# Performance work log

Measured on AMD Instinct MI355X. Metric: run time of the kernel, lower is better.

## Reference

```python
import jax, jax.numpy as jnp
import numpy as np

N_NODES, N_EDGES, N_GRAPHS, H = 20000, 160000, 256, 128
EPS = 1e-5


def setup_inputs() -> dict:
    key = jax.random.key(0)
    it = iter(jax.random.split(key, 64))

    def nk():
        return next(it)

    def lin(fan_in, wshape, bshape):
        s = 1.0 / np.sqrt(fan_in)
        W = jax.random.uniform(nk(), wshape, jnp.float32, -s, s)
        b = jax.random.uniform(nk(), bshape, jnp.float32, -s, s)
        return W, b

    def bn_params(shape):
        g = 1.0 + 0.1 * jax.random.normal(nk(), shape, jnp.float32)
        b = 0.1 * jax.random.normal(nk(), shape, jnp.float32)
        m = 0.1 * jax.random.normal(nk(), shape, jnp.float32)
        v = jax.random.uniform(nk(), shape, jnp.float32, 0.5, 1.5)
        return g, b, m, v

    inp = {}
    inp["x"] = jax.random.normal(nk(), (N_NODES, 10), jnp.float32)
    inp["edge_attr"] = jax.random.normal(nk(), (N_EDGES, 3), jnp.float32)
    inp["edge_index"] = jax.random.randint(nk(), (2, N_EDGES), 0, N_NODES)
    inp["batch"] = jnp.sort(jax.random.randint(nk(), (N_NODES,), 0, N_GRAPHS))
    inp["W_node"], inp["b_node"] = lin(10, (10, H), (H,))
    inp["W_edge"], inp["b_edge"] = lin(3, (3, H), (H,))
    # 10 stacked CGConv layers: lin_f / lin_s each map [2H + H] -> H
    inp["Wf"], inp["bf"] = lin(3 * H, (10, 3 * H, H), (10, H))
    inp["Ws"], inp["bs"] = lin(3 * H, (10, 3 * H, H), (10, H))
    inp["bn_g"], inp["bn_b"], inp["bn_m"], inp["bn_v"] = bn_params((10, H))
    inp["W1"], inp["b1"] = lin(3 * H, (3 * H, 2 * H), (2 * H,))
    inp["bn1_g"], inp["bn1_b"], inp["bn1_m"], inp["bn1_v"] = bn_params((2 * H,))
    inp["W2"], inp["b2"] = lin(2 * H, (2 * H, H), (H,))
    inp["bn2_g"], inp["bn2_b"], inp["bn2_m"], inp["bn2_v"] = bn_params((H,))
    inp["W3"], inp["b3"] = lin(H, (H, H // 2), (H // 2,))
    inp["Wv"], inp["bv"] = lin(H // 2, (H // 2, 1), (1,))
    inp["W_en"], inp["b_en"] = lin(H // 2, (H // 2, 1), (1,))
    inp["Wd"], inp["bd"] = lin(H // 2, (H // 2, 1), (1,))
    inp["Wh"], inp["bh"] = lin(H // 2, (H // 2, 1), (1,))
    return inp


def reference(x, edge_attr, edge_index, batch, W_node, b_node, W_edge, b_edge,
              Wf, bf, Ws, bs, bn_g, bn_b, bn_m, bn_v,
              W1, b1, bn1_g, bn1_b, bn1_m, bn1_v,
              W2, b2, bn2_g, bn2_b, bn2_m, bn2_v,
              W3, b3, Wv, bv, W_en, b_en, Wd, bd, Wh, bh):
    h = jax.nn.relu(x @ W_node + b_node)             # [N, H]
    e = jax.nn.relu(edge_attr @ W_edge + b_edge)     # [E, H]
    src, dst = edge_index[0], edge_index[1]          # PyG: messages src -> dst
    n = h.shape[0]
    for i in range(10):  # fixed layer count, structurally distinct weights
        h_in = h
        z = jnp.concatenate([h[dst], h[src], e], axis=1)          # [E, 3H] = [x_i, x_j, e_ij]
        msg = jax.nn.sigmoid(z @ Wf[i] + bf[i]) * jax.nn.softplus(z @ Ws[i] + bs[i])
        h = h_in + jax.ops.segment_sum(msg, dst, num_segments=n)  # CGConv residual + add-aggr
        h = (h - bn_m[i]) * (bn_g[i] / jnp.sqrt(bn_v[i] + EPS)) + bn_b[i]  # BN (eval)
        h = jax.nn.relu(h)  # dropout is identity in eval
        if i % 2 == 1:
            h = h + h_in
    # global mean / max / add pooling over graphs
    s = jax.ops.segment_sum(h, batch, num_segments=N_GRAPHS)                     # [G, H]
    cnt = jax.ops.segment_sum(jnp.ones((n, 1), h.dtype), batch, num_segments=N_GRAPHS)
    mean = s / jnp.maximum(cnt, 1.0)
    mx = jax.ops.segment_max(h, batch, num_segments=N_GRAPHS)
    g = jnp.concatenate([mean, mx, s], axis=1)                                   # [G, 3H]
    g = jax.nn.relu((g @ W1 + b1 - bn1_m) * (bn1_g / jnp.sqrt(bn1_v + EPS)) + bn1_b)
    g = jax.nn.relu((g @ W2 + b2 - bn2_m) * (bn2_g / jnp.sqrt(bn2_v + EPS)) + bn2_b)
    g = jax.nn.relu(g @ W3 + b3)
    return (g @ Wv + bv, g @ W_en + b_en, g @ Wd + bd, g @ Wh + bh)
```

## Files before the change

### kernel.cpp

```cpp
#include <hip/hip_runtime.h>
#include <hip/hip_bf16.h>
#include <math.h>

#define NN 20000
#define NE 160000
#define NG 256
#define EPSV 1e-5f
#define NQB 2500

typedef short bf16x8 __attribute__((ext_vector_type(8)));
typedef unsigned short u16x8 __attribute__((ext_vector_type(8)));
typedef float f32x4 __attribute__((ext_vector_type(4)));

__device__ __forceinline__ unsigned short f2bf(float f){
  unsigned int u = __float_as_uint(f);
  unsigned int r = (u + 0x7fffu + ((u>>16)&1u)) >> 16;
  return (unsigned short)r;
}
__device__ __forceinline__ float bf2f(unsigned short h){
  return __uint_as_float(((unsigned int)h) << 16);
}
__device__ __forceinline__ float fastmsg(float f, float sv){
  float sg = __builtin_amdgcn_rcpf(1.0f + __expf(-f));
  float sp = fmaxf(sv, 0.0f) + __logf(1.0f + __expf(-fabsf(sv)));
  return sg * sp;
}

__global__ __launch_bounds__(256) void k_hist(const int* __restrict__ ei, int* __restrict__ deg){
  int e = blockIdx.x*256 + threadIdx.x;
  if (e < NE) atomicAdd(&deg[ei[NE+e]], 1);
}
__global__ __launch_bounds__(1024) void k_scan(const int* __restrict__ deg,
                                               int* __restrict__ start, int* __restrict__ cur){
  __shared__ int part[1024];
  int t = threadIdx.x;
  int base = t*20;
  int s = 0;
  for (int j=0;j<20;j++){ int i = base+j; if (i<NN) s += deg[i]; }
  part[t] = s; __syncthreads();
  for (int off=1; off<1024; off<<=1){
    int v = (t >= off) ? part[t-off] : 0;
    __syncthreads();
    part[t] += v;
    __syncthreads();
  }
  int run = (t>0) ? part[t-1] : 0;
  for (int j=0;j<20;j++){
    int i = base+j;
    if (i<NN){ start[i] = run; cur[i] = run; run += deg[i]; }
  }
}
__global__ __launch_bounds__(256) void k_scatter(
    const int* __restrict__ ei, const float* __restrict__ eattr,
    int* __restrict__ cur, int2* __restrict__ esd, float* __restrict__ ea_s){
  int e = blockIdx.x*256 + threadIdx.x;
  if (e >= NE) return;
  int d = ei[NE+e];
  int p = atomicAdd(&cur[d], 1);
  esd[p] = make_int2(ei[e], d);
  ea_s[p*3+0] = eattr[e*3+0];
  ea_s[p*3+1] = eattr[e*3+1];
  ea_s[p*3+2] = eattr[e*3+2];
}

__global__ __launch_bounds__(256) void k_edge_frag(
    const float* __restrict__ ea_s, const float* __restrict__ W_edge,
    const float* __restrict__ b_edge, unsigned short* __restrict__ E_frag)
{
  int idx = blockIdx.x*256 + threadIdx.x;
  if (idx >= 640000) return;
  int g = idx >> 6, l = idx & 63;
  int row = g*16 + (l&15);
  float a0 = ea_s[row*3+0], a1 = ea_s[row*3+1], a2 = ea_s[row*3+2];
  int cbase = (l>>4)*8;
  unsigned short* dst = E_frag + (size_t)g*4096 + l*8;
  #pragma unroll
  for (int ks=0;ks<4;ks++){
    u16x8 hv, lv;
    #pragma unroll
    for (int j=0;j<8;j++){
      int c = cbase + ks*32 + j;
      float v = fmaf(a0, W_edge[c], fmaf(a1, W_edge[128+c], fmaf(a2, W_edge[256+c], b_edge[c])));
      v = fmaxf(v, 0.0f);
      unsigned short hi = f2bf(v);
      hv[j] = hi;
      lv[j] = f2bf(v - bf2f(hi));
    }
    *(u16x8*)(dst + ks*512) = hv;
    *(u16x8*)(dst + 2048 + ks*512) = lv;
  }
}

__global__ __launch_bounds__(256) void k_pack_w(
    const float* __restrict__ Wf, const float* __restrict__ Ws,
    unsigned short* __restrict__ Wpk_hi, unsigned short* __restrict__ Wpk_md,
    unsigned short* __restrict__ Wpk_lo)
{
  int idx = blockIdx.x*256 + threadIdx.x;
  if (idx >= 122880) return;
  int l = idx & 63, ks = (idx>>6)&3, nt = (idx>>8)&7;
  int m = idx >> 11;
  int blk = m % 3, gL = m / 3;
  int g = gL & 1, L = gL >> 1;
  const float* src = (g ? Ws : Wf) + (size_t)L*384*128;
  size_t off = (size_t)m*16384 + (nt*4+ks)*512 + l*8;
  int col = nt*16 + (l&15), k0 = ks*32 + (l>>4)*8;
  #pragma unroll
  for (int j=0;j<8;j++){
    float w = src[(size_t)(blk*128 + k0 + j)*128 + col];
    unsigned short hi = f2bf(w);
    float r1 = w - bf2f(hi);
    unsigned short md = f2bf(r1);
    float r2 = r1 - bf2f(md);
    Wpk_hi[off+j] = hi;
    Wpk_md[off+j] = md;
    Wpk_lo[off+j] = f2bf(r2);
  }
}

__global__ __launch_bounds__(256) void k_embed_node(
    const float* __restrict__ x, const float* __restrict__ W, const float* __restrict__ b,
    float* __restrict__ h, float* __restrict__ hacc)
{
  int i = blockIdx.x*256 + threadIdx.x;
  if (i >= NN*128) return;
  int n = i >> 7, c = i & 127;
  float acc = b[c];
  const float* xr = x + n*10;
  #pragma unroll
  for (int k=0;k<10;k++) acc = fmaf(xr[k], W[k*128+c], acc);
  acc = fmaxf(acc, 0.0f);
  h[i] = acc; hacc[i] = acc;
}

__global__ __launch_bounds__(512,2) void k_nodeproj_mfma(
    const float* __restrict__ h,
    const unsigned short* __restrict__ Wpk_hi, const unsigned short* __restrict__ Wpk_md,
    const unsigned short* __restrict__ Wpk_lo,
    const float* __restrict__ bfv, const float* __restrict__ bsv,
    float* __restrict__ Pd, float* __restrict__ Ps)
{
  __shared__ unsigned short wsm[32768];
  int bid = blockIdx.x;
  int m_idx = bid / 157, nblk = bid - m_idx*157;
  int mm = (m_idx==0)?0:(m_idx==1)?1:(m_idx==2)?3:4;
  int t = threadIdx.x;
  {
    const unsigned short* s0 = Wpk_hi + (size_t)mm*16384;
    const unsigned short* s1 = Wpk_md + (size_t)mm*16384;
    #pragma unroll
    for (int ii=0; ii<4; ii++){
      int o = (t + ii*512)*8;
      *(u16x8*)(wsm + o)         = *(const u16x8*)(s0 + o);
      *(u16x8*)(wsm + 16384 + o) = *(const u16x8*)(s1 + o);
    }
  }
  __syncthreads();
  int l = t & 63, w = t >> 6;
  int nb = nblk*128 + w*16;
  if (nb + 16 > NN) return;
  const float* hb = h + (size_t)(nb + (l&15))*128 + (l>>4)*8;
  bf16x8 ah[4], am[4], al[4];
  #pragma unroll
  for (int ks=0;ks<4;ks++){
    #pragma unroll
    for (int j=0;j<8;j++){
      float v = hb[ks*32 + j];
      unsigned short x0 = f2bf(v);
      float r1 = v - bf2f(x0);
      unsigned short x1 = f2bf(r1);
      float r2 = r1 - bf2f(x1);
      ah[ks][j] = (short)x0; am[ks][j] = (short)x1; al[ks][j] = (short)f2bf(r2);
    }
  }
  const unsigned short* wl = Wpk_lo + (size_t)mm*16384 + l*8;
  float* OUT = (m_idx & 1) ? Ps : Pd;
  int sel = (m_idx >= 2) ? 1 : 0;
  const float* bias = (m_idx==0) ? bfv : (m_idx==2) ? bsv : nullptr;
  int col0 = l & 15, rg = (l>>4)*4;
  #pragma unroll
  for (int nt=0; nt<8; nt++){
    f32x4 c = {0.f,0.f,0.f,0.f};
    #pragma unroll
    for (int ks=0;ks<4;ks++){
      int fo = (nt*4+ks)*512 + l*8;
      bf16x8 bh = *(const bf16x8*)(wsm + fo);
      bf16x8 bm = *(const bf16x8*)(wsm + 16384 + fo);
      bf16x8 bl = *(const bf16x8*)(wl + (nt*4+ks)*512);
      c = __builtin_amdgcn_mfma_f32_16x16x32_bf16(al[ks], bh, c, 0,0,0);
      c = __builtin_amdgcn_mfma_f32_16x16x32_bf16(am[ks], bm, c, 0,0,0);
      c = __builtin_amdgcn_mfma_f32_16x16x32_bf16(ah[ks], bl, c, 0,0,0);
      c = __builtin_amdgcn_mfma_f32_16x16x32_bf16(am[ks], bh, c, 0,0,0);
      c = __builtin_amdgcn_mfma_f32_16x16x32_bf16(ah[ks], bm, c, 0,0,0);
      c = __builtin_amdgcn_mfma_f32_16x16x32_bf16(ah[ks], bh, c, 0,0,0);
    }
    float bb = bias ? bias[nt*16+col0] : 0.0f;
    #pragma unroll
    for (int r=0;r<4;r++)
      OUT[(size_t)(nb+rg+r)*256 + (nt*16+col0)*2 + sel] = c[r] + bb;
  }
}

template<bool PRE>
__global__ __launch_bounds__(256,4) void k_edge_mfma(
    const float* __restrict__ ea_s, const float* __restrict__ W_edge,
    const float* __restrict__ b_edge,
    const unsigned short* __restrict__ E_frag,
    const unsigned short* __restrict__ Wpk_hi,
    const unsigned short* __restrict__ Wpk_md,
    const int2* __restrict__ esd,
    const float* __restrict__ Pd, const float* __restrict__ Ps,
    float* __restrict__ hacc)
{
  __shared__ float wlds[512];
  __shared__ unsigned short bfr[16384];
  int bid = blockIdx.x;
  int q = bid / NQB, eg = bid - q*NQB;
  int t = threadIdx.x;
  if (!PRE)
    for (int i=t;i<512;i+=256) wlds[i] = (i<384)? W_edge[i] : b_edge[i-384];
  #pragma unroll
  for (int ii=0; ii<8; ii++){
    int idx = t + ii*256;
    int f = idx >> 6;
    int off = (idx & 63) * 8;
    int g = f >> 4, term = (f>>3)&1, ntl = (f>>2)&1, ks = f&3;
    const unsigned short* src = (term ? Wpk_md : Wpk_hi)
        + (size_t)(g?5:2)*16384 + (size_t)((((q*2+ntl)*4+ks)*512) + off);
    *(u16x8*)(bfr + f*512 + off) = *(const u16x8*)src;
  }
  __syncthreads();
  int l = t & 63, w = t >> 6;
  int e0 = eg*64;
  bf16x8 ah[4], al[4];
  if (PRE) {
    const unsigned short* ef = E_frag + (size_t)(eg*4 + w)*4096 + l*8;
    #pragma unroll
    for (int ks=0;ks<4;ks++){
      ah[ks] = *(const bf16x8*)(ef + ks*512);
      al[ks] = *(const bf16x8*)(ef + 2048 + ks*512);
    }
  } else {
    int row_edge = e0 + w*16 + (l&15);
    float a0 = ea_s[row_edge*3+0], a1 = ea_s[row_edge*3+1], a2 = ea_s[row_edge*3+2];
    int cbase = (l>>4)*8;
    #pragma unroll
    for (int ks=0;ks<4;ks++){
      #pragma unroll
      for (int j=0;j<8;j++){
        int c = cbase + ks*32 + j;
        float v = fmaf(a0, wlds[c], fmaf(a1, wlds[128+c], fmaf(a2, wlds[256+c], wlds[384+c])));
        v = fmaxf(v, 0.0f);
        unsigned short hi = f2bf(v);
        ah[ks][j] = (short)hi;
        al[ks][j] = (short)f2bf(v - bf2f(hi));
      }
    }
  }
  f32x4 accf[2], accs[2];
  #pragma unroll
  for (int ntl=0; ntl<2; ntl++){
    f32x4 cf = {0.f,0.f,0.f,0.f}, cs = {0.f,0.f,0.f,0.f};
    #pragma unroll
    for (int ks=0; ks<4; ks++){
      bf16x8 bh = *(const bf16x8*)(bfr + ((0<<4)|(0<<3)|(ntl<<2)|ks)*512 + l*8);
      bf16x8 bm = *(const bf16x8*)(bfr + ((0<<4)|(1<<3)|(ntl<<2)|ks)*512 + l*8);
      cf = __builtin_amdgcn_mfma_f32_16x16x32_bf16(ah[ks], bh, cf, 0,0,0);
      cf = __builtin_amdgcn_mfma_f32_16x16x32_bf16(ah[ks], bm, cf, 0,0,0);
      cf = __builtin_amdgcn_mfma_f32_16x16x32_bf16(al[ks], bh, cf, 0,0,0);
      bf16x8 sh = *(const bf16x8*)(bfr + ((1<<4)|(0<<3)|(ntl<<2)|ks)*512 + l*8);
      bf16x8 sm = *(const bf16x8*)(bfr + ((1<<4)|(1<<3)|(ntl<<2)|ks)*512 + l*8);
      cs = __builtin_amdgcn_mfma_f32_16x16x32_bf16(ah[ks], sh, cs, 0,0,0);
      cs = __builtin_amdgcn_mfma_f32_16x16x32_bf16(ah[ks], sm, cs, 0,0,0);
      cs = __builtin_amdgcn_mfma_f32_16x16x32_bf16(al[ks], sh, cs, 0,0,0);
    }
    accf[ntl] = cf; accs[ntl] = cs;
  }
  int eb = e0 + w*16, col0 = l & 15, rg = (l>>4)*4;
  int cA = (q*2+0)*16 + col0;
  int cB = (q*2+1)*16 + col0;
  int prev_d = -1;
  float m0 = 0.f, m1 = 0.f;
  float2 pd0, pd1;
  #pragma unroll
  for (int r=0;r<4;r++){
    int p = eb + rg + r;
    int2 sd = esd[p];
    int s = sd.x, d = sd.y;
    if (d != prev_d){
      if (prev_d >= 0){
        atomicAdd(hacc + (size_t)prev_d*128 + cA, m0);
        atomicAdd(hacc + (size_t)prev_d*128 + cB, m1);
      }
      prev_d = d;
      pd0 = *(const float2*)(Pd + (size_t)d*256 + cA*2);
      pd1 = *(const float2*)(Pd + (size_t)d*256 + cB*2);
      m0 = 0.f; m1 = 0.f;
    }
    float2 ps0 = *(const float2*)(Ps + (size_t)s*256 + cA*2);
    float2 ps1 = *(const float2*)(Ps + (size_t)s*256 + cB*2);
    m0 += fastmsg(accf[0][r] + pd0.x + ps0.x, accs[0][r] + pd0.y + ps0.y);
    m1 += fastmsg(accf[1][r] + pd1.x + ps1.x, accs[1][r] + pd1.y + ps1.y);
  }
  atomicAdd(hacc + (size_t)prev_d*128 + cA, m0);
  atomicAdd(hacc + (size_t)prev_d*128 + cB, m1);
}

__global__ __launch_bounds__(256) void k_bn(
    const float* __restrict__ hacc, const float* __restrict__ hin,
    const float* __restrict__ gam, const float* __restrict__ bet,
    const float* __restrict__ mu, const float* __restrict__ var,
    float* __restrict__ hout, float* __restrict__ haccout, int addres)
{
  int i = blockIdx.x*256 + threadIdx.x;
  if (i >= NN*128) return;
  int c = i & 127;
  float scale = gam[c]*rsqrtf(var[c]+EPSV);
  float tv = (hacc[i]-mu[c])*scale + bet[c];
  tv = fmaxf(tv, 0.0f);
  if (addres) tv += hin[i];
  hout[i] = tv; haccout[i] = tv;
}

__global__ __launch_bounds__(256) void k_pool(
    const float* __restrict__ h, const int* __restrict__ batch,
    float* __restrict__ psum, float* __restrict__ pmax, float* __restrict__ pcnt)
{
  int i = blockIdx.x*256 + threadIdx.x;
  if (i >= NN*128) return;
  int n = i >> 7, c = i & 127;
  int b = batch[n];
  float v = h[i];
  atomicAdd(&psum[b*128+c], v);
  atomicMax((unsigned int*)&pmax[b*128+c], __float_as_uint(v));
  if (c == 0) atomicAdd(&pcnt[b], 1.0f);
}

__global__ __launch_bounds__(256) void k_mlp1(
    const float* __restrict__ psum, const float* __restrict__ pmax, const float* __restrict__ pcnt,
    const float* __restrict__ W1, const float* __restrict__ b1,
    const float* __restrict__ g1g, const float* __restrict__ g1b,
    const float* __restrict__ g1m, const float* __restrict__ g1v,
    float* __restrict__ out)
{
  int i = blockIdx.x*256 + threadIdx.x;
  int g = i >> 8, c = i & 255;
  float inv = 1.0f / fmaxf(pcnt[g], 1.0f);
  float acc = b1[c];
  for (int k=0;k<128;k++) acc = fmaf(psum[g*128+k]*inv, W1[k*256+c], acc);
  for (int k=0;k<128;k++) acc = fmaf(pmax[g*128+k],     W1[(128+k)*256+c], acc);
  for (int k=0;k<128;k++) acc = fmaf(psum[g*128+k],     W1[(256+k)*256+c], acc);
  float scale = g1g[c]*rsqrtf(g1v[c]+EPSV);
  acc = (acc - g1m[c])*scale + g1b[c];
  out[i] = fmaxf(acc, 0.0f);
}

__global__ __launch_bounds__(256) void k_mlp2(
    const float* __restrict__ g1, const float* __restrict__ W2, const float* __restrict__ b2,
    const float* __restrict__ g2g, const float* __restrict__ g2b,
    const float* __restrict__ g2m, const float* __restrict__ g2v,
    float* __restrict__ out)
{
  int i = blockIdx.x*256 + threadIdx.x;
  int g = i >> 7, c = i & 127;
  float acc = b2[c];
  for (int k=0;k<256;k++) acc = fmaf(g1[g*256+k], W2[k*128+c], acc);
  float scale = g2g[c]*rsqrtf(g2v[c]+EPSV);
  acc = (acc - g2m[c])*scale + g2b[c];
  out[i] = fmaxf(acc, 0.0f);
}

__global__ __launch_bounds__(256) void k_mlp3(
    const float* __restrict__ g2, const float* __restrict__ W3, const float* __restrict__ b3,
    float* __restrict__ out)
{
  int i = blockIdx.x*256 + threadIdx.x;
  int g = i >> 6, c = i & 63;
  float acc = b3[c];
  for (int k=0;k<128;k++) acc = fmaf(g2[g*128+k], W3[k*64+c], acc);
  out[i] = fmaxf(acc, 0.0f);
}

__global__ __launch_bounds__(256) void k_heads(
    const float* __restrict__ g3,
    const float* __restrict__ Wv, const float* __restrict__ bv,
    const float* __restrict__ We, const float* __restrict__ be,
    const float* __restrict__ Wd, const float* __restrict__ bd,
    const float* __restrict__ Wh, const float* __restrict__ bh,
    float* __restrict__ out)
{
  int g = blockIdx.x*256 + threadIdx.x;
  if (g >= NG) return;
  float a0=bv[0], a1=be[0], a2=bd[0], a3=bh[0];
  for (int k=0;k<64;k++){
    float xv = g3[g*64+k];
    a0 = fmaf(xv, Wv[k], a0);
    a1 = fmaf(xv, We[k], a1);
    a2 = fmaf(xv, Wd[k], a2);
    a3 = fmaf(xv, Wh[k], a3);
  }
  out[g] = a0; out[NG+g] = a1; out[2*NG+g] = a2; out[3*NG+g] = a3;
}

extern "C" void kernel_launch(void* const* d_in, const int* in_sizes, int n_in,
                              void* d_out, int out_size, void* d_ws, size_t ws_size,
                              hipStream_t stream)
{
  const float* x         = (const float*)d_in[0];
  const float* edge_attr = (const float*)d_in[1];
  const int*   ei        = (const int*)d_in[2];
  const int*   batch     = (const int*)d_in[3];
  const float* W_node    = (const float*)d_in[4];
  const float* b_node    = (const float*)d_in[5];
  const float* W_edge    = (const float*)d_in[6];
  const float* b_edge    = (const float*)d_in[7];
  const float* Wf        = (const float*)d_in[8];
  const float* bf        = (const float*)d_in[9];
  const float* Ws        = (const float*)d_in[10];
  const float* bs        = (const float*)d_in[11];
  const float* bn_g      = (const float*)d_in[12];
  const float* bn_b      = (const float*)d_in[13];
  const float* bn_m      = (const float*)d_in[14];
  const float* bn_v      = (const float*)d_in[15];
  const float* W1        = (const float*)d_in[16];
  const float* b1        = (const float*)d_in[17];
  const float* bn1_g     = (const float*)d_in[18];
  const float* bn1_b     = (const float*)d_in[19];
  const float* bn1_m     = (const float*)d_in[20];
  const float* bn1_v     = (const float*)d_in[21];
  const float* W2        = (const float*)d_in[22];
  const float* b2        = (const float*)d_in[23];
  const float* bn2_g     = (const float*)d_in[24];
  const float* bn2_b     = (const float*)d_in[25];
  const float* bn2_m     = (const float*)d_in[26];
  const float* bn2_v     = (const float*)d_in[27];
  const float* W3        = (const float*)d_in[28];
  const float* b3        = (const float*)d_in[29];
  const float* Wv        = (const float*)d_in[30];
  const float* bv        = (const float*)d_in[31];
  const float* W_en      = (const float*)d_in[32];
  const float* b_en      = (const float*)d_in[33];
  const float* Wd        = (const float*)d_in[34];
  const float* bd        = (const float*)d_in[35];
  const float* Wh        = (const float*)d_in[36];
  const float* bh        = (const float*)d_in[37];

  float* wsf  = (float*)d_ws;
  float* h    = wsf;
  float* hacc = wsf + 2560000;
  float* Pd   = wsf + 5120000;
  float* Ps   = wsf + 10240000;
  unsigned short* Wpk_hi = (unsigned short*)(wsf + 15360000);
  unsigned short* Wpk_md = (unsigned short*)(wsf + 15851520);
  unsigned short* Wpk_lo = (unsigned short*)(wsf + 16343040);
  float* psum = wsf + 16834560;
  float* pmax = psum + 32768;
  float* pcnt = pmax + 32768;
  float* g1   = pcnt + 256;
  float* g2   = g1 + 65536;
  float* g3   = g2 + 32768;
  int*   deg  = (int*)(wsf + 16982272);
  int*   start= deg + 20000;
  int*   cur  = start + 20000;
  int2*  esd  = (int2*)(cur + 20000);
  float* ea_s = (float*)(cur + 20000 + 320000);
  unsigned short* E_frag = (unsigned short*)(wsf + 17842272);
  const size_t need_pre = (size_t)17842272*4 + (size_t)40960000*2;
  const bool PRE = ws_size >= need_pre;

  hipMemsetAsync(deg, 0, 20000*sizeof(int), stream);
  k_hist<<<(NE+255)/256, 256, 0, stream>>>(ei, deg);
  k_scan<<<1, 1024, 0, stream>>>(deg, start, cur);
  k_scatter<<<(NE+255)/256, 256, 0, stream>>>(ei, edge_attr, cur, esd, ea_s);
  if (PRE) k_edge_frag<<<2500, 256, 0, stream>>>(ea_s, W_edge, b_edge, E_frag);

  k_pack_w<<<480, 256, 0, stream>>>(Wf, Ws, Wpk_hi, Wpk_md, Wpk_lo);
  k_embed_node<<<(NN*128+255)/256, 256, 0, stream>>>(x, W_node, b_node, h, hacc);
  hipMemsetAsync(psum, 0, (size_t)(32768+32768+256)*sizeof(float), stream);

  for (int i=0;i<10;i++){
    const unsigned short* WH = Wpk_hi + (size_t)i*6*16384;
    const unsigned short* WM = Wpk_md + (size_t)i*6*16384;
    const unsigned short* WL = Wpk_lo + (size_t)i*6*16384;
    k_nodeproj_mfma<<<628, 512, 0, stream>>>(h, WH, WM, WL,
        bf + i*128, bs + i*128, Pd, Ps);
    if (PRE)
      k_edge_mfma<true><<<4*NQB, 256, 0, stream>>>(ea_s, W_edge, b_edge, E_frag,
          WH, WM, esd, Pd, Ps, hacc);
    else
      k_edge_mfma<false><<<4*NQB, 256, 0, stream>>>(ea_s, W_edge, b_edge, E_frag,
          WH, WM, esd, Pd, Ps, hacc);
    k_bn<<<(NN*128+255)/256, 256, 0, stream>>>(hacc, h,
        bn_g + i*128, bn_b + i*128, bn_m + i*128, bn_v + i*128, h, hacc, i&1);
  }

  k_pool<<<(NN*128+255)/256, 256, 0, stream>>>(h, batch, psum, pmax, pcnt);
  k_mlp1<<<(NG*256)/256, 256, 0, stream>>>(psum, pmax, pcnt, W1, b1, bn1_g, bn1_b, bn1_m, bn1_v, g1);
  k_mlp2<<<(NG*128)/256, 256, 0, stream>>>(g1, W2, b2, bn2_g, bn2_b, bn2_m, bn2_v, g2);
  k_mlp3<<<(NG*64)/256, 256, 0, stream>>>(g2, W3, b3, g3);
  k_heads<<<1, 256, 0, stream>>>(g3, Wv, bv, W_en, b_en, Wd, bd, Wh, bh, (float*)d_out);
}
```

Baseline: 1.439 ms.

## Compute all 128 output columns per edge block, drop LDS weight staging

Each edge block previously handled one quarter of the output columns, so the grid was 4x larger, and it staged a weight slice in shared memory. Now each block covers all 8 column tiles, which removes the duplicate edge-fragment loads, esd reads and dst-segment bookkeeping across quarter blocks. Weight fragments are read directly from global memory (L2-resident) instead of LDS. Launch bounds drop to 3 waves per SIMD to fit the larger accumulator arrays. The risk is more register pressure, lower occupancy, and a grid of only 2500 blocks.

```diff
diff --git a/kernel.cpp b/kernel.cpp
--- a/kernel.cpp
+++ b/kernel.cpp
@@ -202,7 +202,7 @@
 }
 
 template<bool PRE>
-__global__ __launch_bounds__(256,4) void k_edge_mfma(
+__global__ __launch_bounds__(256,3) void k_edge_mfma(
     const float* __restrict__ ea_s, const float* __restrict__ W_edge,
     const float* __restrict__ b_edge,
     const unsigned short* __restrict__ E_frag,
@@ -213,23 +213,12 @@
     float* __restrict__ hacc)
 {
   __shared__ float wlds[512];
-  __shared__ unsigned short bfr[16384];
-  int bid = blockIdx.x;
-  int q = bid / NQB, eg = bid - q*NQB;
   int t = threadIdx.x;
-  if (!PRE)
+  int eg = blockIdx.x;
+  if (!PRE) {
     for (int i=t;i<512;i+=256) wlds[i] = (i<384)? W_edge[i] : b_edge[i-384];
-  #pragma unroll
-  for (int ii=0; ii<8; ii++){
-    int idx = t + ii*256;
-    int f = idx >> 6;
-    int off = (idx & 63) * 8;
-    int g = f >> 4, term = (f>>3)&1, ntl = (f>>2)&1, ks = f&3;
-    const unsigned short* src = (term ? Wpk_md : Wpk_hi)
-        + (size_t)(g?5:2)*16384 + (size_t)((((q*2+ntl)*4+ks)*512) + off);
-    *(u16x8*)(bfr + f*512 + off) = *(const u16x8*)src;
-  }
-  __syncthreads();
+    __syncthreads();
+  }
   int l = t & 63, w = t >> 6;
   int e0 = eg*64;
   bf16x8 ah[4], al[4];
@@ -257,31 +246,34 @@
       }
     }
   }
-  f32x4 accf[2], accs[2];
-  #pragma unroll
-  for (int ntl=0; ntl<2; ntl++){
+  const unsigned short* WHf = Wpk_hi + (size_t)2*16384 + l*8;
+  const unsigned short* WMf = Wpk_md + (size_t)2*16384 + l*8;
+  const unsigned short* WHs = Wpk_hi + (size_t)5*16384 + l*8;
+  const unsigned short* WMs = Wpk_md + (size_t)5*16384 + l*8;
+  f32x4 accf[8], accs[8];
+  #pragma unroll
+  for (int nt=0; nt<8; nt++){
     f32x4 cf = {0.f,0.f,0.f,0.f}, cs = {0.f,0.f,0.f,0.f};
     #pragma unroll
     for (int ks=0; ks<4; ks++){
-      bf16x8 bh = *(const bf16x8*)(bfr + ((0<<4)|(0<<3)|(ntl<<2)|ks)*512 + l*8);
-      bf16x8 bm = *(const bf16x8*)(bfr + ((0<<4)|(1<<3)|(ntl<<2)|ks)*512 + l*8);
+      int fo = (nt*4+ks)*512;
+      bf16x8 bh = *(const bf16x8*)(WHf + fo);
+      bf16x8 bm = *(const bf16x8*)(WMf + fo);
       cf = __builtin_amdgcn_mfma_f32_16x16x32_bf16(ah[ks], bh, cf, 0,0,0);
       cf = __builtin_amdgcn_mfma_f32_16x16x32_bf16(ah[ks], bm, cf, 0,0,0);
       cf = __builtin_amdgcn_mfma_f32_16x16x32_bf16(al[ks], bh, cf, 0,0,0);
-      bf16x8 sh = *(const bf16x8*)(bfr + ((1<<4)|(0<<3)|(ntl<<2)|ks)*512 + l*8);
-      bf16x8 sm = *(const bf16x8*)(bfr + ((1<<4)|(1<<3)|(ntl<<2)|ks)*512 + l*8);
+      bf16x8 sh = *(const bf16x8*)(WHs + fo);
+      bf16x8 sm = *(const bf16x8*)(WMs + fo);
       cs = __builtin_amdgcn_mfma_f32_16x16x32_bf16(ah[ks], sh, cs, 0,0,0);
       cs = __builtin_amdgcn_mfma_f32_16x16x32_bf16(ah[ks], sm, cs, 0,0,0);
       cs = __builtin_amdgcn_mfma_f32_16x16x32_bf16(al[ks], sh, cs, 0,0,0);
     }
-    accf[ntl] = cf; accs[ntl] = cs;
+    accf[nt] = cf; accs[nt] = cs;
   }
   int eb = e0 + w*16, col0 = l & 15, rg = (l>>4)*4;
-  int cA = (q*2+0)*16 + col0;
-  int cB = (q*2+1)*16 + col0;
   int prev_d = -1;
-  float m0 = 0.f, m1 = 0.f;
-  float2 pd0, pd1;
+  float msum[8];
+  float2 pdv[8];
   #pragma unroll
   for (int r=0;r<4;r++){
     int p = eb + rg + r;
@@ -289,21 +281,28 @@
     int s = sd.x, d = sd.y;
     if (d != prev_d){
       if (prev_d >= 0){
-        atomicAdd(hacc + (size_t)prev_d*128 + cA, m0);
-        atomicAdd(hacc + (size_t)prev_d*128 + cB, m1);
+        float* hp = hacc + (size_t)prev_d*128 + col0;
+        #pragma unroll
+        for (int nt=0;nt<8;nt++) atomicAdd(hp + nt*16, msum[nt]);
       }
       prev_d = d;
-      pd0 = *(const float2*)(Pd + (size_t)d*256 + cA*2);
-      pd1 = *(const float2*)(Pd + (size_t)d*256 + cB*2);
-      m0 = 0.f; m1 = 0.f;
-    }
-    float2 ps0 = *(const float2*)(Ps + (size_t)s*256 + cA*2);
-    float2 ps1 = *(const float2*)(Ps + (size_t)s*256 + cB*2);
-    m0 += fastmsg(accf[0][r] + pd0.x + ps0.x, accs[0][r] + pd0.y + ps0.y);
-    m1 += fastmsg(accf[1][r] + pd1.x + ps1.x, accs[1][r] + pd1.y + ps1.y);
-  }
-  atomicAdd(hacc + (size_t)prev_d*128 + cA, m0);
-  atomicAdd(hacc + (size_t)prev_d*128 + cB, m1);
+      const float* pdp = Pd + (size_t)d*256 + col0*2;
+      #pragma unroll
+      for (int nt=0;nt<8;nt++){ pdv[nt] = *(const float2*)(pdp + nt*32); msum[nt] = 0.0f; }
+    }
+    const float* psp = Ps + (size_t)s*256 + col0*2;
+    #pragma unroll
+    for (int nt=0; nt<8; nt++){
+      float2 ps = *(const float2*)(psp + nt*32);
+      msum[nt] += fastmsg(accf[nt][r] + pdv[nt].x + ps.x,
+                          accs[nt][r] + pdv[nt].y + ps.y);
+    }
+  }
+  {
+    float* hp = hacc + (size_t)prev_d*128 + col0;
+    #pragma unroll
+    for (int nt=0;nt<8;nt++) atomicAdd(hp + nt*16, msum[nt]);
+  }
 }
 
 __global__ __launch_bounds__(256) void k_bn(
@@ -485,10 +484,10 @@
     k_nodeproj_mfma<<<628, 512, 0, stream>>>(h, WH, WM, WL,
         bf + i*128, bs + i*128, Pd, Ps);
     if (PRE)
-      k_edge_mfma<true><<<4*NQB, 256, 0, stream>>>(ea_s, W_edge, b_edge, E_frag,
+      k_edge_mfma<true><<<NQB, 256, 0, stream>>>(ea_s, W_edge, b_edge, E_frag,
           WH, WM, esd, Pd, Ps, hacc);
     else
-      k_edge_mfma<false><<<4*NQB, 256, 0, stream>>>(ea_s, W_edge, b_edge, E_frag,
+      k_edge_mfma<false><<<NQB, 256, 0, stream>>>(ea_s, W_edge, b_edge, E_frag,
           WH, WM, esd, Pd, Ps, hacc);
     k_bn<<<(NN*128+255)/256, 256, 0, stream>>>(hacc, h,
         bn_g + i*128, bn_b + i*128, bn_m + i*128, bn_v + i*128, h, hacc, i&1);
```

After: 1.696 ms. 17.9% more time.

## Fuse final BN with pooling, reorder edge block mapping, truncate bf16 splits

Applied to the files above, without the earlier changes.

The last layer's batch-norm is fused into the pooling kernel, which removes one full-size write and read of h. The edge kernel's block index mapping changes so the four column-quarter blocks for the same edge group are adjacent, which should improve L2 reuse of the edge fragments and projection rows. The precomputed edge-fragment loads are also issued before the weight staging and barrier so their latency overlaps. The high bf16 parts of the split-precision decomposition now use truncation instead of rounding, with the residual terms absorbing the difference, which saves ALU work.

```diff
diff --git a/kernel.cpp b/kernel.cpp
--- a/kernel.cpp
+++ b/kernel.cpp
@@ -82,7 +82,7 @@
       int c = cbase + ks*32 + j;
       float v = fmaf(a0, W_edge[c], fmaf(a1, W_edge[128+c], fmaf(a2, W_edge[256+c], b_edge[c])));
       v = fmaxf(v, 0.0f);
-      unsigned short hi = f2bf(v);
+      unsigned short hi = (unsigned short)(__float_as_uint(v) >> 16);
       hv[j] = hi;
       lv[j] = f2bf(v - bf2f(hi));
     }
@@ -166,9 +166,9 @@
     #pragma unroll
     for (int j=0;j<8;j++){
       float v = hb[ks*32 + j];
-      unsigned short x0 = f2bf(v);
+      unsigned short x0 = (unsigned short)(__float_as_uint(v) >> 16);
       float r1 = v - bf2f(x0);
-      unsigned short x1 = f2bf(r1);
+      unsigned short x1 = (unsigned short)(__float_as_uint(r1) >> 16);
       float r2 = r1 - bf2f(x1);
       ah[ks][j] = (short)x0; am[ks][j] = (short)x1; al[ks][j] = (short)f2bf(r2);
     }
@@ -215,10 +215,21 @@
   __shared__ float wlds[512];
   __shared__ unsigned short bfr[16384];
   int bid = blockIdx.x;
-  int q = bid / NQB, eg = bid - q*NQB;
+  int eg = bid >> 2, q = bid & 3;
   int t = threadIdx.x;
-  if (!PRE)
+  int l = t & 63, w = t >> 6;
+  int e0 = eg*64;
+  bf16x8 ah[4], al[4];
+  if (PRE) {
+    const unsigned short* ef = E_frag + (size_t)(eg*4 + w)*4096 + l*8;
+    #pragma unroll
+    for (int ks=0;ks<4;ks++){
+      ah[ks] = *(const bf16x8*)(ef + ks*512);
+      al[ks] = *(const bf16x8*)(ef + 2048 + ks*512);
+    }
+  } else {
     for (int i=t;i<512;i+=256) wlds[i] = (i<384)? W_edge[i] : b_edge[i-384];
+  }
   #pragma unroll
   for (int ii=0; ii<8; ii++){
     int idx = t + ii*256;
@@ -230,17 +241,7 @@
     *(u16x8*)(bfr + f*512 + off) = *(const u16x8*)src;
   }
   __syncthreads();
-  int l = t & 63, w = t >> 6;
-  int e0 = eg*64;
-  bf16x8 ah[4], al[4];
-  if (PRE) {
-    const unsigned short* ef = E_frag + (size_t)(eg*4 + w)*4096 + l*8;
-    #pragma unroll
-    for (int ks=0;ks<4;ks++){
-      ah[ks] = *(const bf16x8*)(ef + ks*512);
-      al[ks] = *(const bf16x8*)(ef + 2048 + ks*512);
-    }
-  } else {
+  if (!PRE) {
     int row_edge = e0 + w*16 + (l&15);
     float a0 = ea_s[row_edge*3+0], a1 = ea_s[row_edge*3+1], a2 = ea_s[row_edge*3+2];
     int cbase = (l>>4)*8;
@@ -251,7 +252,7 @@
         int c = cbase + ks*32 + j;
         float v = fmaf(a0, wlds[c], fmaf(a1, wlds[128+c], fmaf(a2, wlds[256+c], wlds[384+c])));
         v = fmaxf(v, 0.0f);
-        unsigned short hi = f2bf(v);
+        unsigned short hi = (unsigned short)(__float_as_uint(v) >> 16);
         ah[ks][j] = (short)hi;
         al[ks][j] = (short)f2bf(v - bf2f(hi));
       }
@@ -322,17 +323,24 @@
   hout[i] = tv; haccout[i] = tv;
 }
 
-__global__ __launch_bounds__(256) void k_pool(
-    const float* __restrict__ h, const int* __restrict__ batch,
-    float* __restrict__ psum, float* __restrict__ pmax, float* __restrict__ pcnt)
+__global__ __launch_bounds__(256) void k_bn_pool(
+    const float* __restrict__ hacc, const float* __restrict__ hin,
+    const float* __restrict__ gam, const float* __restrict__ bet,
+    const float* __restrict__ mu, const float* __restrict__ var,
+    const int* __restrict__ batch,
+    float* __restrict__ psum, float* __restrict__ pmax, float* __restrict__ pcnt,
+    int addres)
 {
   int i = blockIdx.x*256 + threadIdx.x;
   if (i >= NN*128) return;
   int n = i >> 7, c = i & 127;
+  float scale = gam[c]*rsqrtf(var[c]+EPSV);
+  float tv = (hacc[i]-mu[c])*scale + bet[c];
+  tv = fmaxf(tv, 0.0f);
+  if (addres) tv += hin[i];
   int b = batch[n];
-  float v = h[i];
-  atomicAdd(&psum[b*128+c], v);
-  atomicMax((unsigned int*)&pmax[b*128+c], __float_as_uint(v));
+  atomicAdd(&psum[b*128+c], tv);
+  atomicMax((unsigned int*)&pmax[b*128+c], __float_as_uint(tv));
   if (c == 0) atomicAdd(&pcnt[b], 1.0f);
 }
 
@@ -490,11 +498,15 @@
     else
       k_edge_mfma<false><<<4*NQB, 256, 0, stream>>>(ea_s, W_edge, b_edge, E_frag,
           WH, WM, esd, Pd, Ps, hacc);
-    k_bn<<<(NN*128+255)/256, 256, 0, stream>>>(hacc, h,
-        bn_g + i*128, bn_b + i*128, bn_m + i*128, bn_v + i*128, h, hacc, i&1);
-  }
-
-  k_pool<<<(NN*128+255)/256, 256, 0, stream>>>(h, batch, psum, pmax, pcnt);
+    if (i < 9)
+      k_bn<<<(NN*128+255)/256, 256, 0, stream>>>(hacc, h,
+          bn_g + i*128, bn_b + i*128, bn_m + i*128, bn_v + i*128, h, hacc, i&1);
+    else
+      k_bn_pool<<<(NN*128+255)/256, 256, 0, stream>>>(hacc, h,
+          bn_g + i*128, bn_b + i*128, bn_m + i*128, bn_v + i*128,
+          batch, psum, pmax, pcnt, i&1);
+  }
+
   k_mlp1<<<(NG*256)/256, 256, 0, stream>>>(psum, pmax, pcnt, W1, b1, bn1_g, bn1_b, bn1_m, bn1_v, g1);
   k_mlp2<<<(NG*128)/256, 256, 0, stream>>>(g1, W2, b2, bn2_g, bn2_b, bn2_m, bn2_v, g2);
   k_mlp3<<<(NG*64)/256, 256, 0, stream>>>(g2, W3, b3, g3);
```

Measured after the change: 1.364 ms. 1.05x faster.
